# Optimization experiments

Hardware: AMD Instinct MI355X
Metric: run time of the kernel (lower is better)

Reference implementation:

```python
import jax, jax.numpy as jnp
from jax import lax
import numpy as np

NUM_CAPS = 4
CAP_DIM = 8
NUM_CLASSES = 10
CLASS_DIM = 16


def squash(x):
    # x: [..., D]; scale = |x|^2/(1+|x|^2)/sqrt(|x|^2+1e-8)
    sq = jnp.sum(x * x, axis=-1, keepdims=True)
    return sq / (1.0 + sq) / jnp.sqrt(sq + 1e-8) * x


def primary_caps(x, w, b):
    # x: [B,C,H,W], w: [32,C,3,3] -> caps [B, H*W*NUM_CAPS, CAP_DIM]
    out = lax.conv_general_dilated(
        x, w, window_strides=(1, 1), padding=[(1, 1), (1, 1)],
        dimension_numbers=('NCHW', 'OIHW', 'NCHW')) + b[None, :, None, None]
    B, C, H, W = out.shape
    out = out.reshape(B, NUM_CAPS, CAP_DIM, H * W)
    out = out.transpose(0, 3, 1, 2).reshape(B, H * W * NUM_CAPS, CAP_DIM)
    return squash(out)


def setup_inputs() -> dict:
    key = jax.random.key(0)
    ks = jax.random.split(key, 7)
    B, H, Wd = 64, 32, 32
    hsi_c, sar_c = 144, 4
    N = 2 * H * Wd * NUM_CAPS  # 8192
    return {
        'x_hsi': jax.random.normal(ks[0], (B, hsi_c, H, Wd), jnp.float32),
        'x_sar': jax.random.normal(ks[1], (B, sar_c, H, Wd), jnp.float32),
        'wh': jax.random.normal(ks[2], (NUM_CAPS * CAP_DIM, hsi_c, 3, 3), jnp.float32) * 0.05,
        'bh': jax.random.normal(ks[3], (NUM_CAPS * CAP_DIM,), jnp.float32) * 0.05,
        'ws': jax.random.normal(ks[4], (NUM_CAPS * CAP_DIM, sar_c, 3, 3), jnp.float32) * 0.05,
        'bs': jax.random.normal(ks[5], (NUM_CAPS * CAP_DIM,), jnp.float32) * 0.05,
        'W': jax.random.normal(ks[6], (N, NUM_CLASSES, CLASS_DIM, CAP_DIM), jnp.float32),
    }


def reference(x_hsi, x_sar, wh, bh, ws, bs, W):
    caps_h = primary_caps(x_hsi, wh, bh)
    caps_s = primary_caps(x_sar, ws, bs)
    caps = jnp.concatenate([caps_h, caps_s], axis=1)  # [B, N, D]
    N = caps.shape[1]
    # routing_iters=1 with b=0 => c = 1/N uniform; s = sum_n c*u_hat = mean_n u_hat
    # u_hat[b,n,c,j] = sum_d W[n,c,j,d] * caps[b,n,d] (fused, never materialized)
    s = jnp.einsum('bnd,ncjd->bcj', caps, W) / N  # [B, num_classes, class_dim]
    v = squash(s)
    logits = jnp.sqrt(jnp.sum(v * v, axis=-1))  # [B, num_classes]
    return logits
```

## Files before the change

### kernel.cpp

```cpp
#include <hip/hip_runtime.h>
#include <hip/hip_bf16.h>


typedef __attribute__((ext_vector_type(8))) short bf16x8s;
typedef __attribute__((ext_vector_type(4))) float f32x4;

__device__ inline short f2bf(float f) {
    __hip_bfloat16 h = __float2bfloat16(f);
    return *reinterpret_cast<short*>(&h);
}

__global__ __launch_bounds__(256) void prep_kernel(
        const float* __restrict__ wh, short* __restrict__ wtb,
        const float* __restrict__ x_hsi, short* __restrict__ xb,
        const float* __restrict__ wsar, float* __restrict__ wt_s) {
    __shared__ short tile[160 * 33];
    int t = threadIdx.x;
    if (blockIdx.x < 180) {
        int idx = blockIdx.x * 256 + t;
        int tap = idx / 5120;
        int rest = idx - tap * 5120;
        int oc = rest / 160;
        int cin = rest - oc * 160;
        short v = 0;
        if (cin < 144) v = f2bf(wh[(oc * 144 + cin) * 9 + tap]);
        wtb[idx] = v;
        return;
    }
    if (blockIdx.x == 2228) {
        for (int idx = t; idx < 1152; idx += 256) {
            int oc = idx & 31;
            int rest = idx >> 5;
            int tap = rest % 9;
            int cin = rest / 9;
            wt_s[cin * 288 + tap * 32 + oc] = wsar[(oc * 4 + cin) * 9 + tap];
        }
        return;
    }
    int blk = blockIdx.x - 180;
    int b = blk >> 5;
    int y = blk & 31;
    for (int idx = t; idx < 512; idx += 256) {
        int x = idx & 31, cin = 144 + (idx >> 5);
        tile[cin * 33 + x] = 0;
    }
    for (int base = 0; base < 144; base += 8) {
        int cin = base + (t >> 5), x = t & 31;
        float v = x_hsi[(((size_t)b * 144 + cin) * 32 + y) * 32 + x];
        tile[cin * 33 + x] = f2bf(v);
    }
    __syncthreads();
    unsigned* dst = (unsigned*)(xb + ((size_t)(b * 32 + y) * 32) * 160);
    for (int idx = t; idx < 2560; idx += 256) {
        int x = idx / 80;
        int cinp = idx - x * 80;
        unsigned lo = (unsigned short)tile[(2 * cinp) * 33 + x];
        unsigned hi = (unsigned short)tile[(2 * cinp + 1) * 33 + x];
        dst[idx] = lo | (hi << 16);
    }
}

__global__ __launch_bounds__(256) void conv_both_kernel(
        const float* __restrict__ x_sar, const short* __restrict__ xb,
        const short* __restrict__ wtb, const float* __restrict__ bh,
        const float* __restrict__ wt_s, const float* __restrict__ bs,
        short* __restrict__ capsb) {
    __shared__ union {
        float ct[64][34];
        float red[4][32][64];
    } sm;
    int t = threadIdx.x;

    if (blockIdx.x < 1024) {
        int l = t & 63;
        int wv = t >> 6;
        int mhalf = wv >> 1;
        int nt = wv & 1;
        int l15 = l & 15, lhi = l >> 4;
        int b = blockIdx.x >> 4;
        int y0 = (blockIdx.x & 15) << 1;
        int y = y0 + mhalf;
        int kofs = lhi * 8;

        const short* xbb = xb + (size_t)b * 1024 * 160;

        f32x4 acc0 = {0.f, 0.f, 0.f, 0.f};
        f32x4 acc1 = {0.f, 0.f, 0.f, 0.f};
        const bf16x8s zf = {0, 0, 0, 0, 0, 0, 0, 0};

        #pragma unroll
        for (int tap = 0; tap < 9; ++tap) {
            int dy = tap / 3, dx = tap % 3;
            int iy = y + dy - 1;
            bool rowok = (unsigned)iy < 32u;
            int iyc = rowok ? iy : 0;
            int ix0 = l15 + dx - 1;
            int ix1 = 16 + l15 + dx - 1;
            bool ok0 = rowok && ((unsigned)ix0 < 32u);
            bool ok1 = rowok && ((unsigned)ix1 < 32u);
            int ix0c = min(max(ix0, 0), 31);
            int ix1c = min(max(ix1, 0), 31);
            const short* xa0 = xbb + ((size_t)(iyc * 32 + ix0c)) * 160 + kofs;
            const short* xa1 = xbb + ((size_t)(iyc * 32 + ix1c)) * 160 + kofs;
            const short* wa = wtb + ((size_t)tap * 32 + nt * 16 + l15) * 160 + kofs;
            #pragma unroll
            for (int kc = 0; kc < 5; ++kc) {
                bf16x8s bfrag = *(const bf16x8s*)(wa + kc * 32);
                bf16x8s a0 = *(const bf16x8s*)(xa0 + kc * 32);
                bf16x8s a1 = *(const bf16x8s*)(xa1 + kc * 32);
                a0 = ok0 ? a0 : zf;
                a1 = ok1 ? a1 : zf;
                acc0 = __builtin_amdgcn_mfma_f32_16x16x32_bf16(a0, bfrag, acc0, 0, 0, 0);
                acc1 = __builtin_amdgcn_mfma_f32_16x16x32_bf16(a1, bfrag, acc1, 0, 0, 0);
            }
        }

        #pragma unroll
        for (int r = 0; r < 4; ++r) {
            sm.ct[mhalf * 32 + lhi * 4 + r][nt * 16 + l15] = acc0[r];
            sm.ct[mhalf * 32 + 16 + lhi * 4 + r][nt * 16 + l15] = acc1[r];
        }
        __syncthreads();

        int p = t >> 2;
        int cap = t & 3;
        float s[8];
        float sq = 0.0f;
        #pragma unroll
        for (int d = 0; d < 8; ++d) {
            s[d] = sm.ct[p][cap * 8 + d] + bh[cap * 8 + d];
            sq += s[d] * s[d];
        }
        float scale = sq / ((1.0f + sq) * sqrtf(sq + 1e-8f));
        int pix = (y0 + (p >> 5)) * 32 + (p & 31);
        int n = pix * 4 + cap;
        bf16x8s o;
        #pragma unroll
        for (int d = 0; d < 8; ++d) o[d] = f2bf(s[d] * scale);
        *(bf16x8s*)(capsb + ((size_t)b * 8192 + n) * 8) = o;
    } else {
        int bidx = blockIdx.x - 1024;
        int b = bidx >> 4;
        int wave = __builtin_amdgcn_readfirstlane(t >> 6);
        int lane = t & 63;
        int x = lane & 31;
        int yy = lane >> 5;
        int y = ((bidx & 15) << 1) + yy;

        const float* xc = x_sar + ((size_t)b * 4 + wave) * 1024;
        const float* wc = wt_s + wave * 288;

        float acc[32];
        #pragma unroll
        for (int oc = 0; oc < 32; ++oc) acc[oc] = 0.0f;

        #pragma unroll
        for (int ky = 0; ky < 3; ++ky) {
            int iy = y + ky - 1;
            bool rowok = (iy >= 0) && (iy < 32);
            const float* xrow = xc + iy * 32;
            float v0 = (rowok && x > 0)  ? xrow[x - 1] : 0.0f;
            float v1 = rowok             ? xrow[x]     : 0.0f;
            float v2 = (rowok && x < 31) ? xrow[x + 1] : 0.0f;
            const float* wk = wc + ky * 96;
            #pragma unroll
            for (int oc = 0; oc < 32; ++oc)
                acc[oc] += v0 * wk[oc] + v1 * wk[32 + oc] + v2 * wk[64 + oc];
        }

        #pragma unroll
        for (int oc = 0; oc < 32; ++oc) sm.red[wave][oc][lane] = acc[oc];
        __syncthreads();

        int cap = t >> 6;
        int p = t & 63;
        float s[8];
        float sq = 0.0f;
        #pragma unroll
        for (int d = 0; d < 8; ++d) {
            int oc = cap * 8 + d;
            s[d] = bs[oc] + sm.red[0][oc][p] + sm.red[1][oc][p]
                          + sm.red[2][oc][p] + sm.red[3][oc][p];
            sq += s[d] * s[d];
        }
        float scale = sq / ((1.0f + sq) * sqrtf(sq + 1e-8f));
        int pix = (((bidx & 15) << 1) + (p >> 5)) * 32 + (p & 31);
        int n = 4096 + pix * 4 + cap;
        bf16x8s o;
        #pragma unroll
        for (int d = 0; d < 8; ++d) o[d] = f2bf(s[d] * scale);
        *(bf16x8s*)(capsb + ((size_t)b * 8192 + n) * 8) = o;
    }
}

__global__ __launch_bounds__(256) void routing_mfma_kernel(
        const short* __restrict__ capsb, const float* __restrict__ W,
        float* __restrict__ partials) {
    __shared__ union {
        short ct[64][64][8];
        float red[4][64][34];
    } sm;
    int t = threadIdx.x;
    int kc = blockIdx.x;
    int ntp = blockIdx.y;
    int n0 = kc * 64;

    {
        int b = t >> 2;
        int ng = t & 3;
        const short* src = capsb + ((size_t)b * 8192 + n0 + ng * 16) * 8;
        #pragma unroll
        for (int i = 0; i < 16; ++i) {
            bf16x8s v = *(const bf16x8s*)(src + i * 8);
            *(bf16x8s*)&sm.ct[ng * 16 + i][b][0] = v;
        }
    }
    __syncthreads();

    int l = t & 63;
    int wv = t >> 6;
    int l15 = l & 15, lhi = l >> 4;

    f32x4 acc[2][4];
    #pragma unroll
    for (int a = 0; a < 2; ++a)
        #pragma unroll
        for (int m = 0; m < 4; ++m) acc[a][m] = (f32x4){0.f, 0.f, 0.f, 0.f};

    #pragma unroll
    for (int ks = 0; ks < 4; ++ks) {
        int nl = (wv * 4 + ks) * 4 + lhi;
        int n = n0 + nl;
        const float* wp = W + ((size_t)n * 160 + ntp * 32 + l15) * 8;
        union { short s[8]; bf16x8s v; } bu[2];
        #pragma unroll
        for (int ntl = 0; ntl < 2; ++ntl) {
            const float* wq = wp + (size_t)ntl * 128;
            float4 w0 = *(const float4*)wq;
            float4 w1 = *(const float4*)(wq + 4);
            bu[ntl].s[0] = f2bf(w0.x); bu[ntl].s[1] = f2bf(w0.y);
            bu[ntl].s[2] = f2bf(w0.z); bu[ntl].s[3] = f2bf(w0.w);
            bu[ntl].s[4] = f2bf(w1.x); bu[ntl].s[5] = f2bf(w1.y);
            bu[ntl].s[6] = f2bf(w1.z); bu[ntl].s[7] = f2bf(w1.w);
        }
        bf16x8s af[4];
        #pragma unroll
        for (int mt = 0; mt < 4; ++mt)
            af[mt] = *(const bf16x8s*)&sm.ct[nl][mt * 16 + l15][0];
        #pragma unroll
        for (int ntl = 0; ntl < 2; ++ntl)
            #pragma unroll
            for (int mt = 0; mt < 4; ++mt)
                acc[ntl][mt] = __builtin_amdgcn_mfma_f32_16x16x32_bf16(
                    af[mt], bu[ntl].v, acc[ntl][mt], 0, 0, 0);
    }
    __syncthreads();

    #pragma unroll
    for (int ntl = 0; ntl < 2; ++ntl)
        #pragma unroll
        for (int mt = 0; mt < 4; ++mt)
            #pragma unroll
            for (int r = 0; r < 4; ++r)
                sm.red[wv][mt * 16 + lhi * 4 + r][ntl * 16 + l15] = acc[ntl][mt][r];
    __syncthreads();

    for (int idx = t; idx < 2048; idx += 256) {
        int b = idx >> 5, cjl = idx & 31;
        float sum = sm.red[0][b][cjl] + sm.red[1][b][cjl]
                  + sm.red[2][b][cjl] + sm.red[3][b][cjl];
        partials[(((size_t)kc * 5 + ntp) * 64 + b) * 32 + cjl] = sum;
    }
}

__global__ __launch_bounds__(256) void finalize_kernel(
        const float* __restrict__ partials, float* __restrict__ out) {
    __shared__ float s_sh[160];
    int t = threadIdx.x;
    int b = blockIdx.x;
    if (t < 160) {
        int ntp = t >> 5, cjl = t & 31;
        float s = 0.0f;
        #pragma unroll 8
        for (int kc = 0; kc < 128; ++kc)
            s += partials[(((size_t)kc * 5 + ntp) * 64 + b) * 32 + cjl];
        s_sh[ntp * 32 + cjl] = s * (1.0f / 8192.0f);
    }
    __syncthreads();
    if (t < 10) {
        float sq = 0.0f;
        #pragma unroll
        for (int j = 0; j < 16; ++j) {
            float v = s_sh[t * 16 + j];
            sq += v * v;
        }
        float scale = sq / ((1.0f + sq) * sqrtf(sq + 1e-8f));
        out[b * 10 + t] = sqrtf(sq) * scale;
    }
}

extern "C" void kernel_launch(void* const* d_in, const int* in_sizes, int n_in,
                              void* d_out, int out_size, void* d_ws, size_t ws_size,
                              hipStream_t stream) {
    const float* x_hsi = (const float*)d_in[0];
    const float* x_sar = (const float*)d_in[1];
    const float* wh    = (const float*)d_in[2];
    const float* bh    = (const float*)d_in[3];
    const float* wsar  = (const float*)d_in[4];
    const float* bs    = (const float*)d_in[5];
    const float* W     = (const float*)d_in[6];
    float* out = (float*)d_out;

    char* ws = (char*)d_ws;
    short* wtb      = (short*)(ws + 0);
    float* wt_s     = (float*)(ws + 98304);
    short* xb       = (short*)(ws + 131072);
    short* capsb    = (short*)(ws + 21102592);
    float* partials = (float*)(ws + 29491200);

    prep_kernel<<<2229, 256, 0, stream>>>(wh, wtb, x_hsi, xb, wsar, wt_s);

    conv_both_kernel<<<2048, 256, 0, stream>>>(x_sar, xb, wtb, bh, wt_s, bs, capsb);

    routing_mfma_kernel<<<dim3(128, 5), 256, 0, stream>>>(capsb, W, partials);

    finalize_kernel<<<64, 256, 0, stream>>>(partials, out);
}
```

Measured before the change: 76.43 us.

## Use padded channel-blocked input layout, per-pixel SAR conv, finer routing split

The HSI input is repacked into a zero-padded 34x34 layout blocked by 8 channels, and the weights get a matching layout. This drops bounds checks and clamping from the MFMA conv loop and makes the A/B fragment loads contiguous per 8-channel block. The SAR conv now gives each thread one pixel with all 4 input channels, removing the shared-memory cross-wave reduction and cutting its blocks from 1024 to 256. Routing uses 32 capsules per block with twice as many blocks, which doubles the partials the finalize kernel must sum, and the partials buffer reuses the xb2 workspace region.

```diff
diff --git a/kernel.cpp b/kernel.cpp
--- a/kernel.cpp
+++ b/kernel.cpp
@@ -10,24 +10,28 @@
     return *reinterpret_cast<short*>(&h);
 }
 
+#define XPLANE 1156
+#define XB_B (20 * XPLANE * 8)
+
 __global__ __launch_bounds__(256) void prep_kernel(
-        const float* __restrict__ wh, short* __restrict__ wtb,
-        const float* __restrict__ x_hsi, short* __restrict__ xb,
+        const float* __restrict__ wh, short* __restrict__ wtb2,
+        const float* __restrict__ x_hsi, short* __restrict__ xb2,
         const float* __restrict__ wsar, float* __restrict__ wt_s) {
-    __shared__ short tile[160 * 33];
     int t = threadIdx.x;
     if (blockIdx.x < 180) {
         int idx = blockIdx.x * 256 + t;
         int tap = idx / 5120;
-        int rest = idx - tap * 5120;
-        int oc = rest / 160;
-        int cin = rest - oc * 160;
+        int r2 = idx - tap * 5120;
+        int cb = r2 >> 8;
+        int oc = (r2 >> 3) & 31;
+        int d = r2 & 7;
+        int ch = cb * 8 + d;
         short v = 0;
-        if (cin < 144) v = f2bf(wh[(oc * 144 + cin) * 9 + tap]);
-        wtb[idx] = v;
+        if (ch < 144) v = f2bf(wh[(oc * 144 + ch) * 9 + tap]);
+        wtb2[idx] = v;
         return;
     }
-    if (blockIdx.x == 2228) {
+    if (blockIdx.x == 2356) {
         for (int idx = t; idx < 1152; idx += 256) {
             int oc = idx & 31;
             int rest = idx >> 5;
@@ -38,37 +42,33 @@
         return;
     }
     int blk = blockIdx.x - 180;
-    int b = blk >> 5;
-    int y = blk & 31;
-    for (int idx = t; idx < 512; idx += 256) {
-        int x = idx & 31, cin = 144 + (idx >> 5);
-        tile[cin * 33 + x] = 0;
-    }
-    for (int base = 0; base < 144; base += 8) {
-        int cin = base + (t >> 5), x = t & 31;
-        float v = x_hsi[(((size_t)b * 144 + cin) * 32 + y) * 32 + x];
-        tile[cin * 33 + x] = f2bf(v);
-    }
-    __syncthreads();
-    unsigned* dst = (unsigned*)(xb + ((size_t)(b * 32 + y) * 32) * 160);
-    for (int idx = t; idx < 2560; idx += 256) {
-        int x = idx / 80;
-        int cinp = idx - x * 80;
-        unsigned lo = (unsigned short)tile[(2 * cinp) * 33 + x];
-        unsigned hi = (unsigned short)tile[(2 * cinp + 1) * 33 + x];
-        dst[idx] = lo | (hi << 16);
+    int b = blk / 34;
+    int y_o = blk - b * 34;
+    bool yok = (y_o >= 1) && (y_o <= 32);
+    int iy = y_o - 1;
+    short* dstb = xb2 + (size_t)b * XB_B;
+    for (int item = t; item < 680; item += 256) {
+        int cb = item / 34;
+        int xx = item - cb * 34;
+        bf16x8s v = {0, 0, 0, 0, 0, 0, 0, 0};
+        if (yok && xx >= 1 && xx <= 32 && cb < 18) {
+            int x = xx - 1;
+            #pragma unroll
+            for (int d = 0; d < 8; ++d) {
+                int ch = cb * 8 + d;
+                v[d] = f2bf(x_hsi[(((size_t)b * 144 + ch) * 32 + iy) * 32 + x]);
+            }
+        }
+        *(bf16x8s*)(dstb + ((size_t)(cb * 34 + y_o) * 34 + xx) * 8) = v;
     }
 }
 
 __global__ __launch_bounds__(256) void conv_both_kernel(
-        const float* __restrict__ x_sar, const short* __restrict__ xb,
-        const short* __restrict__ wtb, const float* __restrict__ bh,
+        const float* __restrict__ x_sar, const short* __restrict__ xb2,
+        const short* __restrict__ wtb2, const float* __restrict__ bh,
         const float* __restrict__ wt_s, const float* __restrict__ bs,
         short* __restrict__ capsb) {
-    __shared__ union {
-        float ct[64][34];
-        float red[4][32][64];
-    } sm;
+    __shared__ float ct[64][34];
     int t = threadIdx.x;
 
     if (blockIdx.x < 1024) {
@@ -80,45 +80,32 @@
         int b = blockIdx.x >> 4;
         int y0 = (blockIdx.x & 15) << 1;
         int y = y0 + mhalf;
-        int kofs = lhi * 8;
-
-        const short* xbb = xb + (size_t)b * 1024 * 160;
+
+        const short* xaBase = xb2 + (size_t)b * XB_B + (size_t)lhi * XPLANE * 8;
+        const short* waBase = wtb2 + (size_t)lhi * 256 + (size_t)(nt * 16 + l15) * 8;
 
         f32x4 acc0 = {0.f, 0.f, 0.f, 0.f};
         f32x4 acc1 = {0.f, 0.f, 0.f, 0.f};
-        const bf16x8s zf = {0, 0, 0, 0, 0, 0, 0, 0};
 
         #pragma unroll
         for (int tap = 0; tap < 9; ++tap) {
             int dy = tap / 3, dx = tap % 3;
-            int iy = y + dy - 1;
-            bool rowok = (unsigned)iy < 32u;
-            int iyc = rowok ? iy : 0;
-            int ix0 = l15 + dx - 1;
-            int ix1 = 16 + l15 + dx - 1;
-            bool ok0 = rowok && ((unsigned)ix0 < 32u);
-            bool ok1 = rowok && ((unsigned)ix1 < 32u);
-            int ix0c = min(max(ix0, 0), 31);
-            int ix1c = min(max(ix1, 0), 31);
-            const short* xa0 = xbb + ((size_t)(iyc * 32 + ix0c)) * 160 + kofs;
-            const short* xa1 = xbb + ((size_t)(iyc * 32 + ix1c)) * 160 + kofs;
-            const short* wa = wtb + ((size_t)tap * 32 + nt * 16 + l15) * 160 + kofs;
+            int pixoff = ((y + dy) * 34 + l15 + dx) * 8;
             #pragma unroll
             for (int kc = 0; kc < 5; ++kc) {
-                bf16x8s bfrag = *(const bf16x8s*)(wa + kc * 32);
-                bf16x8s a0 = *(const bf16x8s*)(xa0 + kc * 32);
-                bf16x8s a1 = *(const bf16x8s*)(xa1 + kc * 32);
-                a0 = ok0 ? a0 : zf;
-                a1 = ok1 ? a1 : zf;
-                acc0 = __builtin_amdgcn_mfma_f32_16x16x32_bf16(a0, bfrag, acc0, 0, 0, 0);
-                acc1 = __builtin_amdgcn_mfma_f32_16x16x32_bf16(a1, bfrag, acc1, 0, 0, 0);
+                const short* xa = xaBase + (size_t)kc * (4 * XPLANE * 8) + pixoff;
+                bf16x8s a0 = *(const bf16x8s*)xa;
+                bf16x8s a1 = *(const bf16x8s*)(xa + 16 * 8);
+                bf16x8s bf = *(const bf16x8s*)(waBase + (size_t)(tap * 20 + kc * 4) * 256);
+                acc0 = __builtin_amdgcn_mfma_f32_16x16x32_bf16(a0, bf, acc0, 0, 0, 0);
+                acc1 = __builtin_amdgcn_mfma_f32_16x16x32_bf16(a1, bf, acc1, 0, 0, 0);
             }
         }
 
         #pragma unroll
         for (int r = 0; r < 4; ++r) {
-            sm.ct[mhalf * 32 + lhi * 4 + r][nt * 16 + l15] = acc0[r];
-            sm.ct[mhalf * 32 + 16 + lhi * 4 + r][nt * 16 + l15] = acc1[r];
+            ct[mhalf * 32 + lhi * 4 + r][nt * 16 + l15] = acc0[r];
+            ct[mhalf * 32 + 16 + lhi * 4 + r][nt * 16 + l15] = acc1[r];
         }
         __syncthreads();
 
@@ -128,7 +115,7 @@
         float sq = 0.0f;
         #pragma unroll
         for (int d = 0; d < 8; ++d) {
-            s[d] = sm.ct[p][cap * 8 + d] + bh[cap * 8 + d];
+            s[d] = ct[p][cap * 8 + d] + bh[cap * 8 + d];
             sq += s[d] * s[d];
         }
         float scale = sq / ((1.0f + sq) * sqrtf(sq + 1e-8f));
@@ -139,57 +126,45 @@
         for (int d = 0; d < 8; ++d) o[d] = f2bf(s[d] * scale);
         *(bf16x8s*)(capsb + ((size_t)b * 8192 + n) * 8) = o;
     } else {
-        int bidx = blockIdx.x - 1024;
-        int b = bidx >> 4;
-        int wave = __builtin_amdgcn_readfirstlane(t >> 6);
-        int lane = t & 63;
-        int x = lane & 31;
-        int yy = lane >> 5;
-        int y = ((bidx & 15) << 1) + yy;
-
-        const float* xc = x_sar + ((size_t)b * 4 + wave) * 1024;
-        const float* wc = wt_s + wave * 288;
+        int px_global = (blockIdx.x - 1024) * 256 + t;
+        int b = px_global >> 10;
+        int p = px_global & 1023;
+        int y = p >> 5, x = p & 31;
 
         float acc[32];
         #pragma unroll
-        for (int oc = 0; oc < 32; ++oc) acc[oc] = 0.0f;
-
-        #pragma unroll
-        for (int ky = 0; ky < 3; ++ky) {
-            int iy = y + ky - 1;
-            bool rowok = (iy >= 0) && (iy < 32);
-            const float* xrow = xc + iy * 32;
-            float v0 = (rowok && x > 0)  ? xrow[x - 1] : 0.0f;
-            float v1 = rowok             ? xrow[x]     : 0.0f;
-            float v2 = (rowok && x < 31) ? xrow[x + 1] : 0.0f;
-            const float* wk = wc + ky * 96;
-            #pragma unroll
-            for (int oc = 0; oc < 32; ++oc)
-                acc[oc] += v0 * wk[oc] + v1 * wk[32 + oc] + v2 * wk[64 + oc];
-        }
-
-        #pragma unroll
-        for (int oc = 0; oc < 32; ++oc) sm.red[wave][oc][lane] = acc[oc];
-        __syncthreads();
-
-        int cap = t >> 6;
-        int p = t & 63;
-        float s[8];
-        float sq = 0.0f;
-        #pragma unroll
-        for (int d = 0; d < 8; ++d) {
-            int oc = cap * 8 + d;
-            s[d] = bs[oc] + sm.red[0][oc][p] + sm.red[1][oc][p]
-                          + sm.red[2][oc][p] + sm.red[3][oc][p];
-            sq += s[d] * s[d];
-        }
-        float scale = sq / ((1.0f + sq) * sqrtf(sq + 1e-8f));
-        int pix = (((bidx & 15) << 1) + (p >> 5)) * 32 + (p & 31);
-        int n = 4096 + pix * 4 + cap;
-        bf16x8s o;
-        #pragma unroll
-        for (int d = 0; d < 8; ++d) o[d] = f2bf(s[d] * scale);
-        *(bf16x8s*)(capsb + ((size_t)b * 8192 + n) * 8) = o;
+        for (int oc = 0; oc < 32; ++oc) acc[oc] = bs[oc];
+
+        for (int cin = 0; cin < 4; ++cin) {
+            const float* xc = x_sar + ((size_t)b * 4 + cin) * 1024;
+            const float* wc = wt_s + cin * 288;
+            #pragma unroll
+            for (int ky = 0; ky < 3; ++ky) {
+                int iy = y + ky - 1;
+                bool rowok = (iy >= 0) && (iy < 32);
+                const float* xrow = xc + iy * 32;
+                float v0 = (rowok && x > 0)  ? xrow[x - 1] : 0.0f;
+                float v1 = rowok             ? xrow[x]     : 0.0f;
+                float v2 = (rowok && x < 31) ? xrow[x + 1] : 0.0f;
+                const float* wk = wc + ky * 96;
+                #pragma unroll
+                for (int oc = 0; oc < 32; ++oc)
+                    acc[oc] += v0 * wk[oc] + v1 * wk[32 + oc] + v2 * wk[64 + oc];
+            }
+        }
+
+        #pragma unroll
+        for (int cap = 0; cap < 4; ++cap) {
+            float sq = 0.0f;
+            #pragma unroll
+            for (int d = 0; d < 8; ++d) sq += acc[cap * 8 + d] * acc[cap * 8 + d];
+            float scale = sq / ((1.0f + sq) * sqrtf(sq + 1e-8f));
+            int n = 4096 + p * 4 + cap;
+            bf16x8s o;
+            #pragma unroll
+            for (int d = 0; d < 8; ++d) o[d] = f2bf(acc[cap * 8 + d] * scale);
+            *(bf16x8s*)(capsb + ((size_t)b * 8192 + n) * 8) = o;
+        }
     }
 }
 
@@ -197,22 +172,22 @@
         const short* __restrict__ capsb, const float* __restrict__ W,
         float* __restrict__ partials) {
     __shared__ union {
-        short ct[64][64][8];
-        float red[4][64][34];
+        short ct[32][64][8];
+        float red[4][64][32];
     } sm;
     int t = threadIdx.x;
     int kc = blockIdx.x;
     int ntp = blockIdx.y;
-    int n0 = kc * 64;
+    int n0 = kc * 32;
 
     {
         int b = t >> 2;
         int ng = t & 3;
-        const short* src = capsb + ((size_t)b * 8192 + n0 + ng * 16) * 8;
-        #pragma unroll
-        for (int i = 0; i < 16; ++i) {
+        const short* src = capsb + ((size_t)b * 8192 + n0 + ng * 8) * 8;
+        #pragma unroll
+        for (int i = 0; i < 8; ++i) {
             bf16x8s v = *(const bf16x8s*)(src + i * 8);
-            *(bf16x8s*)&sm.ct[ng * 16 + i][b][0] = v;
+            *(bf16x8s*)&sm.ct[ng * 8 + i][b][0] = v;
         }
     }
     __syncthreads();
@@ -228,8 +203,8 @@
         for (int m = 0; m < 4; ++m) acc[a][m] = (f32x4){0.f, 0.f, 0.f, 0.f};
 
     #pragma unroll
-    for (int ks = 0; ks < 4; ++ks) {
-        int nl = (wv * 4 + ks) * 4 + lhi;
+    for (int ks = 0; ks < 2; ++ks) {
+        int nl = (wv * 2 + ks) * 4 + lhi;
         int n = n0 + nl;
         const float* wp = W + ((size_t)n * 160 + ntp * 32 + l15) * 8;
         union { short s[8]; bf16x8s v; } bu[2];
@@ -282,7 +257,7 @@
         int ntp = t >> 5, cjl = t & 31;
         float s = 0.0f;
         #pragma unroll 8
-        for (int kc = 0; kc < 128; ++kc)
+        for (int kc = 0; kc < 256; ++kc)
             s += partials[(((size_t)kc * 5 + ntp) * 64 + b) * 32 + cjl];
         s_sh[ntp * 32 + cjl] = s * (1.0f / 8192.0f);
     }
@@ -312,17 +287,17 @@
     float* out = (float*)d_out;
 
     char* ws = (char*)d_ws;
-    short* wtb      = (short*)(ws + 0);
+    short* wtb2     = (short*)(ws + 0);
     float* wt_s     = (float*)(ws + 98304);
-    short* xb       = (short*)(ws + 131072);
-    short* capsb    = (short*)(ws + 21102592);
-    float* partials = (float*)(ws + 29491200);
-
-    prep_kernel<<<2229, 256, 0, stream>>>(wh, wtb, x_hsi, xb, wsar, wt_s);
-
-    conv_both_kernel<<<2048, 256, 0, stream>>>(x_sar, xb, wtb, bh, wt_s, bs, capsb);
-
-    routing_mfma_kernel<<<dim3(128, 5), 256, 0, stream>>>(capsb, W, partials);
+    short* xb2      = (short*)(ws + 131072);
+    float* partials = (float*)(ws + 131072);
+    short* capsb    = (short*)(ws + 23805952);
+
+    prep_kernel<<<2357, 256, 0, stream>>>(wh, wtb2, x_hsi, xb2, wsar, wt_s);
+
+    conv_both_kernel<<<1280, 256, 0, stream>>>(x_sar, xb2, wtb2, bh, wt_s, bs, capsb);
+
+    routing_mfma_kernel<<<dim3(256, 5), 256, 0, stream>>>(capsb, W, partials);
 
     finalize_kernel<<<64, 256, 0, stream>>>(partials, out);
 }
```

Result: no change. 77.78 us (+1.8%).
